# Optimization experiments

Hardware: AMD Instinct MI355X
Metric: run time of the kernel (lower is better)

## Reference

```python
import jax, jax.numpy as jnp
import numpy as np


def setup_inputs() -> dict:
    key = jax.random.key(0)
    k1, k2, k3 = jax.random.split(key, 3)
    B, N, D = 16, 2048, 128
    q = jax.random.normal(k1, (B, N, D), dtype=jnp.float32)
    k = jax.random.normal(k2, (B, D, N), dtype=jnp.float32)
    v = jax.random.normal(k3, (B, N, D), dtype=jnp.float32)
    return {"q": q, "k": k, "v": v}


def reference(q, k, v):
    # scores: [B, N, N] — note NO 1/sqrt(d) scaling, matching the source
    scores = jnp.einsum('bnd,bdm->bnm', q, k)
    probs = jax.nn.softmax(scores, axis=-1)
    out = jnp.einsum('bnm,bmd->bnd', probs, v)  # [B, N, D]
    return out
```

## Files before the change

kernel.cpp:

```cpp
#include <hip/hip_runtime.h>
#include <hip/hip_bf16.h>


typedef __attribute__((ext_vector_type(8))) _Float16 f16x8;
typedef __attribute__((ext_vector_type(16))) float f32x16;

constexpr int Bz = 16;
constexpr int Nn = 2048;
constexpr int Dd = 128;
constexpr int BM = 128;
constexpr int BN = 32;
constexpr int PK = 40;

__device__ __forceinline__ int swz(int r) { return (r ^ (r >> 3)) & 7; }
__device__ __forceinline__ int sw4(int d) { return ((d >> 1) ^ (d >> 3)) & 3; }

__device__ __forceinline__ uint packh2(float a, float b) {
    union { _Float16 h[2]; uint u; } p;
    p.h[0] = (_Float16)a; p.h[1] = (_Float16)b;
    return p.u;
}

__global__ __launch_bounds__(512, 2)
void fattn_kernel(const float* __restrict__ qg,
                  const float* __restrict__ kg,
                  const float* __restrict__ vg,
                  float* __restrict__ og)
{
    __shared__ ushort lds_k[2][BN * Dd];
    __shared__ ushort lds_v[2][Dd * BN];
    __shared__ ushort lds_p[4][32 * PK];

    const int bid  = blockIdx.x;
    const int xcd  = bid & 7;
    const int idx  = bid >> 3;
    const int b    = xcd * 2 + (idx >> 4);
    const int q0   = (idx & 15) * BM;
    const int tid  = threadIdx.x;
    const int wv   = tid >> 6;
    const int lane = tid & 63;
    const int h    = lane >> 5;
    const int l31  = lane & 31;
    const bool producer = (wv >= 4);

    const int ptid = (wv - 4) * 64 + lane;
    const int kgrp = ptid & 3;
    const int krow = ptid >> 2;
    const int vgrp = ptid & 15;
    const int vrow = ptid >> 4;
    const float* kbase = kg + (size_t)b * Dd * Nn;
    const float* vbase = vg + (size_t)b * Nn * Dd;
    float4 kr[4], vr[4];

    auto issue_loads = [&](int n0) {
        const int d0 = krow * 2;
        const float* s0 = kbase + (size_t)d0 * Nn + n0 + kgrp * 8;
        kr[0] = ((const float4*)s0)[0];
        kr[1] = ((const float4*)s0)[1];
        kr[2] = ((const float4*)(s0 + Nn))[0];
        kr[3] = ((const float4*)(s0 + Nn))[1];
        const int kk0 = vrow * 2;
        const float* t0 = vbase + (size_t)(n0 + kk0) * Dd + vgrp * 8;
        vr[0] = ((const float4*)t0)[0];
        vr[1] = ((const float4*)t0)[1];
        vr[2] = ((const float4*)(t0 + Dd))[0];
        vr[3] = ((const float4*)(t0 + Dd))[1];
    };
    auto write_lds = [&](int buf) {
        uint* kw = (uint*)lds_k[buf];
        const float* av = (const float*)&kr[0];
        const float* bv = (const float*)&kr[2];
        #pragma unroll
        for (int j = 0; j < 8; ++j) {
            const int n = kgrp * 8 + j;
            kw[n * (Dd / 2) + (krow ^ (swz(n) << 2))] = packh2(av[j], bv[j]);
        }
        uint* vw = (uint*)lds_v[buf];
        const float* cv = (const float*)&vr[0];
        const float* dv = (const float*)&vr[2];
        #pragma unroll
        for (int j = 0; j < 8; ++j) {
            const int dd = vgrp * 8 + j;
            vw[dd * (BN / 2) + (vrow ^ (sw4(dd) << 2))] = packh2(cv[j], dv[j]);
        }
    };

    f16x8 qf[8];
    if (!producer) {
        const float* qp = qg + (size_t)(b * Nn + q0 + wv * 32 + l31) * Dd + h * 8;
        #pragma unroll
        for (int c = 0; c < 8; ++c) {
            float4 x0 = *(const float4*)(qp + c * 16);
            float4 x1 = *(const float4*)(qp + c * 16 + 4);
            const float xv[8] = {x0.x, x0.y, x0.z, x0.w, x1.x, x1.y, x1.z, x1.w};
            union { f16x8 v; _Float16 e[8]; } u;
            #pragma unroll
            for (int j = 0; j < 8; ++j) u.e[j] = (_Float16)xv[j];
            qf[c] = u.v;
        }
    }
    f32x16 accO[4];
    #pragma unroll
    for (int dt = 0; dt < 4; ++dt)
        #pragma unroll
        for (int r = 0; r < 16; ++r) accO[dt][r] = 0.f;
    float m_i = -1e30f, l_i = 0.f;

    if (producer) {
        issue_loads(0);
        write_lds(0);
    }
    __syncthreads();

    constexpr int ITERS = Nn / BN;
    for (int it = 0; it < ITERS; ++it) {
        const int cur = it & 1;
        if (producer) {
            if (it + 1 < ITERS) {
                issue_loads((it + 1) * BN);
                write_lds(cur ^ 1);
            }
        } else {
            const ushort* kb = lds_k[cur];
            const ushort* vb = lds_v[cur];

            f32x16 accS;
            #pragma unroll
            for (int r = 0; r < 16; ++r) accS[r] = 0.f;
            {
                const int kkrow = l31;
                const int sw = swz(kkrow) << 3;
                #pragma unroll
                for (int c = 0; c < 8; ++c) {
                    f16x8 kf = *(const f16x8*)&kb[kkrow * Dd + ((c * 16 + h * 8) ^ sw)];
                    accS = __builtin_amdgcn_mfma_f32_32x32x16_f16(kf, qf[c], accS, 0, 0, 0);
                }
            }

            float mx = accS[0];
            #pragma unroll
            for (int r = 1; r < 16; ++r) mx = fmaxf(mx, accS[r]);
            mx = fmaxf(mx, __shfl_xor(mx, 32, 64));
            const float mn = fmaxf(m_i, mx);
            const float alpha = __expf(m_i - mn);
            m_i = mn;
            float local = 0.f;
            #pragma unroll
            for (int r = 0; r < 16; ++r) {
                const float p = __expf(accS[r] - mn);
                accS[r] = p;
                local += p;
            }
            l_i = l_i * alpha + local;
            #pragma unroll
            for (int dt = 0; dt < 4; ++dt)
                #pragma unroll
                for (int r = 0; r < 16; ++r) accO[dt][r] *= alpha;

            ushort* pl = lds_p[wv];
            #pragma unroll
            for (int g = 0; g < 4; ++g) {
                uint2 w;
                w.x = packh2(accS[4 * g + 0], accS[4 * g + 1]);
                w.y = packh2(accS[4 * g + 2], accS[4 * g + 3]);
                *(uint2*)(pl + l31 * PK + 8 * g + 4 * h) = w;
            }
            f16x8 pf0 = *(const f16x8*)&pl[l31 * PK + 8 * h];
            f16x8 pf1 = *(const f16x8*)&pl[l31 * PK + 16 + 8 * h];

            #pragma unroll
            for (int dt = 0; dt < 4; ++dt) {
                const int drow = dt * 32 + l31;
                const int sv = sw4(drow) << 3;
                f16x8 vf0 = *(const f16x8*)&vb[drow * BN + ((8 * h) ^ sv)];
                f16x8 vf1 = *(const f16x8*)&vb[drow * BN + ((16 + 8 * h) ^ sv)];
                accO[dt] = __builtin_amdgcn_mfma_f32_32x32x16_f16(vf0, pf0, accO[dt], 0, 0, 0);
                accO[dt] = __builtin_amdgcn_mfma_f32_32x32x16_f16(vf1, pf1, accO[dt], 0, 0, 0);
            }
        }
        __syncthreads();
    }

    if (!producer) {
        float l = l_i + __shfl_xor(l_i, 32, 64);
        const float inv = 1.f / l;
        float* ob = og + (size_t)(b * Nn + q0 + wv * 32 + l31) * Dd;
        #pragma unroll
        for (int dt = 0; dt < 4; ++dt) {
            #pragma unroll
            for (int g = 0; g < 4; ++g) {
                float4 val;
                val.x = accO[dt][4 * g + 0] * inv;
                val.y = accO[dt][4 * g + 1] * inv;
                val.z = accO[dt][4 * g + 2] * inv;
                val.w = accO[dt][4 * g + 3] * inv;
                *(float4*)(ob + dt * 32 + 8 * g + 4 * h) = val;
            }
        }
    }
}

extern "C" void kernel_launch(void* const* d_in, const int* in_sizes, int n_in,
                              void* d_out, int out_size, void* d_ws, size_t ws_size,
                              hipStream_t stream) {
    const float* q = (const float*)d_in[0];
    const float* k = (const float*)d_in[1];
    const float* v = (const float*)d_in[2];
    float* o = (float*)d_out;
    (void)d_ws; (void)ws_size; (void)in_sizes; (void)n_in; (void)out_size;
    fattn_kernel<<<dim3(Bz * (Nn / BM)), dim3(512), 0, stream>>>(q, k, v, o);
}
```

Baseline: 143.6 us.

## Register-prefetch K/V two tiles ahead, shuffle P in registers, lazy rescale with exp2

The producer waves now keep two register sets of K/V, so each global load is issued one iteration before its LDS write, hiding more memory latency. The consumer drops the LDS round trip for P and builds the MFMA B operand with cross-half shuffles. Q is prescaled by log2(e) so exp2 can be used directly. The online-softmax rescale of O and l is skipped unless the running max grows by more than 8 (in log2 units), and fp32-to-fp16 packing uses cvt_pkrtz. It also adds setprio around the MFMA blocks and a tree max reduction, at the cost of more registers and round-toward-zero rounding on the fp16 operands.

```diff
diff --git a/kernel.cpp b/kernel.cpp
--- a/kernel.cpp
+++ b/kernel.cpp
@@ -1,5 +1,4 @@
 #include <hip/hip_runtime.h>
-#include <hip/hip_bf16.h>
 
 
 typedef __attribute__((ext_vector_type(8))) _Float16 f16x8;
@@ -10,15 +9,16 @@
 constexpr int Dd = 128;
 constexpr int BM = 128;
 constexpr int BN = 32;
-constexpr int PK = 40;
 
 __device__ __forceinline__ int swz(int r) { return (r ^ (r >> 3)) & 7; }
 __device__ __forceinline__ int sw4(int d) { return ((d >> 1) ^ (d >> 3)) & 3; }
 
-__device__ __forceinline__ uint packh2(float a, float b) {
-    union { _Float16 h[2]; uint u; } p;
-    p.h[0] = (_Float16)a; p.h[1] = (_Float16)b;
-    return p.u;
+__device__ __forceinline__ uint pkrtz(float a, float b) {
+    return __builtin_bit_cast(uint, __builtin_amdgcn_cvt_pkrtz(a, b));
+}
+
+__device__ __forceinline__ float exp2i(float x) {
+    return __builtin_amdgcn_exp2f(x);
 }
 
 __global__ __launch_bounds__(512, 2)
@@ -29,7 +29,6 @@
 {
     __shared__ ushort lds_k[2][BN * Dd];
     __shared__ ushort lds_v[2][Dd * BN];
-    __shared__ ushort lds_p[4][32 * PK];
 
     const int bid  = blockIdx.x;
     const int xcd  = bid & 7;
@@ -50,9 +49,9 @@
     const int vrow = ptid >> 4;
     const float* kbase = kg + (size_t)b * Dd * Nn;
     const float* vbase = vg + (size_t)b * Nn * Dd;
-    float4 kr[4], vr[4];
-
-    auto issue_loads = [&](int n0) {
+    float4 kr0[4], vr0[4], kr1[4], vr1[4];
+
+    auto issue_loads = [&](int n0, float4 (&kr)[4], float4 (&vr)[4]) {
         const int d0 = krow * 2;
         const float* s0 = kbase + (size_t)d0 * Nn + n0 + kgrp * 8;
         kr[0] = ((const float4*)s0)[0];
@@ -66,14 +65,14 @@
         vr[2] = ((const float4*)(t0 + Dd))[0];
         vr[3] = ((const float4*)(t0 + Dd))[1];
     };
-    auto write_lds = [&](int buf) {
+    auto write_lds = [&](int buf, const float4 (&kr)[4], const float4 (&vr)[4]) {
         uint* kw = (uint*)lds_k[buf];
         const float* av = (const float*)&kr[0];
         const float* bv = (const float*)&kr[2];
         #pragma unroll
         for (int j = 0; j < 8; ++j) {
             const int n = kgrp * 8 + j;
-            kw[n * (Dd / 2) + (krow ^ (swz(n) << 2))] = packh2(av[j], bv[j]);
+            kw[n * (Dd / 2) + (krow ^ (swz(n) << 2))] = pkrtz(av[j], bv[j]);
         }
         uint* vw = (uint*)lds_v[buf];
         const float* cv = (const float*)&vr[0];
@@ -81,7 +80,7 @@
         #pragma unroll
         for (int j = 0; j < 8; ++j) {
             const int dd = vgrp * 8 + j;
-            vw[dd * (BN / 2) + (vrow ^ (sw4(dd) << 2))] = packh2(cv[j], dv[j]);
+            vw[dd * (BN / 2) + (vrow ^ (sw4(dd) << 2))] = pkrtz(cv[j], dv[j]);
         }
     };
 
@@ -95,7 +94,8 @@
             const float xv[8] = {x0.x, x0.y, x0.z, x0.w, x1.x, x1.y, x1.z, x1.w};
             union { f16x8 v; _Float16 e[8]; } u;
             #pragma unroll
-            for (int j = 0; j < 8; ++j) u.e[j] = (_Float16)xv[j];
+            for (int j = 0; j < 8; ++j)
+                u.e[j] = (_Float16)(xv[j] * 1.44269504088896340736f);
             qf[c] = u.v;
         }
     }
@@ -106,77 +106,116 @@
         for (int r = 0; r < 16; ++r) accO[dt][r] = 0.f;
     float m_i = -1e30f, l_i = 0.f;
 
-    if (producer) {
-        issue_loads(0);
-        write_lds(0);
-    }
-    __syncthreads();
-
-    constexpr int ITERS = Nn / BN;
-    for (int it = 0; it < ITERS; ++it) {
-        const int cur = it & 1;
-        if (producer) {
-            if (it + 1 < ITERS) {
-                issue_loads((it + 1) * BN);
-                write_lds(cur ^ 1);
+    auto consume = [&](const ushort* kb, const ushort* vb) {
+        f32x16 accS;
+        #pragma unroll
+        for (int r = 0; r < 16; ++r) accS[r] = 0.f;
+        {
+            const int kkrow = l31;
+            const int sw = swz(kkrow) << 3;
+            __builtin_amdgcn_s_setprio(1);
+            #pragma unroll
+            for (int c = 0; c < 8; ++c) {
+                f16x8 kf = *(const f16x8*)&kb[kkrow * Dd + ((c * 16 + h * 8) ^ sw)];
+                accS = __builtin_amdgcn_mfma_f32_32x32x16_f16(kf, qf[c], accS, 0, 0, 0);
             }
-        } else {
-            const ushort* kb = lds_k[cur];
-            const ushort* vb = lds_v[cur];
-
-            f32x16 accS;
-            #pragma unroll
-            for (int r = 0; r < 16; ++r) accS[r] = 0.f;
-            {
-                const int kkrow = l31;
-                const int sw = swz(kkrow) << 3;
-                #pragma unroll
-                for (int c = 0; c < 8; ++c) {
-                    f16x8 kf = *(const f16x8*)&kb[kkrow * Dd + ((c * 16 + h * 8) ^ sw)];
-                    accS = __builtin_amdgcn_mfma_f32_32x32x16_f16(kf, qf[c], accS, 0, 0, 0);
-                }
-            }
-
-            float mx = accS[0];
-            #pragma unroll
-            for (int r = 1; r < 16; ++r) mx = fmaxf(mx, accS[r]);
-            mx = fmaxf(mx, __shfl_xor(mx, 32, 64));
+            __builtin_amdgcn_s_setprio(0);
+        }
+
+        f16x8 vf[4][2];
+        #pragma unroll
+        for (int dt = 0; dt < 4; ++dt) {
+            const int drow = dt * 32 + l31;
+            const int sv = sw4(drow) << 3;
+            vf[dt][0] = *(const f16x8*)&vb[drow * BN + ((8 * h) ^ sv)];
+            vf[dt][1] = *(const f16x8*)&vb[drow * BN + ((16 + 8 * h) ^ sv)];
+        }
+
+        float t0 = fmaxf(accS[0], accS[1]),  t1 = fmaxf(accS[2], accS[3]);
+        float t2 = fmaxf(accS[4], accS[5]),  t3 = fmaxf(accS[6], accS[7]);
+        float t4 = fmaxf(accS[8], accS[9]),  t5 = fmaxf(accS[10], accS[11]);
+        float t6 = fmaxf(accS[12], accS[13]), t7 = fmaxf(accS[14], accS[15]);
+        float u0 = fmaxf(t0, t1), u1 = fmaxf(t2, t3);
+        float u2 = fmaxf(t4, t5), u3 = fmaxf(t6, t7);
+        float mx = fmaxf(fmaxf(u0, u1), fmaxf(u2, u3));
+        mx = fmaxf(mx, __shfl_xor(mx, 32, 64));
+
+        if (!__all(mx <= m_i + 8.f)) {
             const float mn = fmaxf(m_i, mx);
-            const float alpha = __expf(m_i - mn);
+            const float al = exp2i(m_i - mn);
             m_i = mn;
-            float local = 0.f;
-            #pragma unroll
-            for (int r = 0; r < 16; ++r) {
-                const float p = __expf(accS[r] - mn);
-                accS[r] = p;
-                local += p;
-            }
-            l_i = l_i * alpha + local;
+            l_i *= al;
             #pragma unroll
             for (int dt = 0; dt < 4; ++dt)
                 #pragma unroll
-                for (int r = 0; r < 16; ++r) accO[dt][r] *= alpha;
-
-            ushort* pl = lds_p[wv];
-            #pragma unroll
-            for (int g = 0; g < 4; ++g) {
-                uint2 w;
-                w.x = packh2(accS[4 * g + 0], accS[4 * g + 1]);
-                w.y = packh2(accS[4 * g + 2], accS[4 * g + 3]);
-                *(uint2*)(pl + l31 * PK + 8 * g + 4 * h) = w;
-            }
-            f16x8 pf0 = *(const f16x8*)&pl[l31 * PK + 8 * h];
-            f16x8 pf1 = *(const f16x8*)&pl[l31 * PK + 16 + 8 * h];
-
-            #pragma unroll
-            for (int dt = 0; dt < 4; ++dt) {
-                const int drow = dt * 32 + l31;
-                const int sv = sw4(drow) << 3;
-                f16x8 vf0 = *(const f16x8*)&vb[drow * BN + ((8 * h) ^ sv)];
-                f16x8 vf1 = *(const f16x8*)&vb[drow * BN + ((16 + 8 * h) ^ sv)];
-                accO[dt] = __builtin_amdgcn_mfma_f32_32x32x16_f16(vf0, pf0, accO[dt], 0, 0, 0);
-                accO[dt] = __builtin_amdgcn_mfma_f32_32x32x16_f16(vf1, pf1, accO[dt], 0, 0, 0);
-            }
+                for (int r = 0; r < 16; ++r) accO[dt][r] *= al;
+        }
+        float local = 0.f;
+        #pragma unroll
+        for (int r = 0; r < 16; ++r) {
+            const float p = exp2i(accS[r] - m_i);
+            accS[r] = p;
+            local += p;
+        }
+        l_i += local;
+
+        const uint pA0 = pkrtz(accS[0],  accS[1]);
+        const uint pA1 = pkrtz(accS[2],  accS[3]);
+        const uint pB0 = pkrtz(accS[4],  accS[5]);
+        const uint pB1 = pkrtz(accS[6],  accS[7]);
+        const uint pC0 = pkrtz(accS[8],  accS[9]);
+        const uint pC1 = pkrtz(accS[10], accS[11]);
+        const uint pD0 = pkrtz(accS[12], accS[13]);
+        const uint pD1 = pkrtz(accS[14], accS[15]);
+        const uint yA0 = __shfl_xor(pA0, 32, 64);
+        const uint yA1 = __shfl_xor(pA1, 32, 64);
+        const uint yB0 = __shfl_xor(pB0, 32, 64);
+        const uint yB1 = __shfl_xor(pB1, 32, 64);
+        const uint yC0 = __shfl_xor(pC0, 32, 64);
+        const uint yC1 = __shfl_xor(pC1, 32, 64);
+        const uint yD0 = __shfl_xor(pD0, 32, 64);
+        const uint yD1 = __shfl_xor(pD1, 32, 64);
+        union { uint u[4]; f16x8 v; } P0, P1;
+        P0.u[0] = h ? yB0 : pA0;
+        P0.u[1] = h ? yB1 : pA1;
+        P0.u[2] = h ? pB0 : yA0;
+        P0.u[3] = h ? pB1 : yA1;
+        P1.u[0] = h ? yD0 : pC0;
+        P1.u[1] = h ? yD1 : pC1;
+        P1.u[2] = h ? pD0 : yC0;
+        P1.u[3] = h ? pD1 : yC1;
+        const f16x8 pf0 = P0.v, pf1 = P1.v;
+
+        __builtin_amdgcn_s_setprio(1);
+        #pragma unroll
+        for (int dt = 0; dt < 4; ++dt) {
+            accO[dt] = __builtin_amdgcn_mfma_f32_32x32x16_f16(vf[dt][0], pf0, accO[dt], 0, 0, 0);
+            accO[dt] = __builtin_amdgcn_mfma_f32_32x32x16_f16(vf[dt][1], pf1, accO[dt], 0, 0, 0);
+        }
+        __builtin_amdgcn_s_setprio(0);
+    };
+
+    if (producer) {
+        issue_loads(0,  kr0, vr0);
+        issue_loads(BN, kr1, vr1);
+        write_lds(0, kr0, vr0);
+    }
+    __syncthreads();
+
+    constexpr int ITERS = Nn / BN;
+    for (int it = 0; it < ITERS; it += 2) {
+        if (producer) {
+            write_lds(1, kr1, vr1);
+            if (it + 2 < ITERS) issue_loads((it + 2) * BN, kr0, vr0);
+        } else {
+            consume(lds_k[0], lds_v[0]);
+        }
+        __syncthreads();
+        if (producer) {
+            if (it + 2 < ITERS) write_lds(0, kr0, vr0);
+            if (it + 3 < ITERS) issue_loads((it + 3) * BN, kr1, vr1);
+        } else {
+            consume(lds_k[1], lds_v[1]);
         }
         __syncthreads();
     }
```

New measurement: 133.5 us. 7.1% less time.
